# Kernel optimization log

Measured on AMD Instinct MI355X. Metric: run time of the kernel, lower is better.

The kernel has to match this reference:

```python
import jax, jax.numpy as jnp
import numpy as np

H = 16  # hidden size


def _gru_dir(x_tbi, Wih, Whh, bih, bhh, reverse):
    """Single-direction GRU over time. x_tbi: [T,B,I]. Returns [T,B,H] outputs
    aligned to original time positions (lax.scan reverse matches torch's
    bidirectional alignment). PyTorch gate order: r, z, n."""
    B = x_tbi.shape[1]
    h0 = jnp.zeros((B, Whh.shape[1]), x_tbi.dtype)
    # Precompute all input projections in one big GEMM: [T,B,3H]
    gi_all = jnp.einsum('tbi,gi->tbg', x_tbi, Wih) + bih

    def step(h, gi):
        gh = h @ Whh.T + bhh                     # [B,3H]
        i_r, i_z, i_n = jnp.split(gi, 3, axis=-1)
        h_r, h_z, h_n = jnp.split(gh, 3, axis=-1)
        r = jax.nn.sigmoid(i_r + h_r)
        z = jax.nn.sigmoid(i_z + h_z)
        n = jnp.tanh(i_n + r * h_n)
        h_new = (1.0 - z) * n + z * h
        return h_new, h_new

    _, ys = jax.lax.scan(step, h0, gi_all, reverse=reverse)
    return ys  # [T,B,H]


def _bigru_layer(x_tbi, pf, pb):
    yf = _gru_dir(x_tbi, pf[0], pf[1], pf[2], pf[3], False)
    yb = _gru_dir(x_tbi, pb[0], pb[1], pb[2], pb[3], True)
    return jnp.concatenate([yf, yb], axis=-1)  # [T,B,2H]


def setup_inputs() -> dict:
    key = jax.random.key(0)
    ks = jax.random.split(key, 20)
    B, T, I = 4096, 512, 1
    bound = 1.0 / np.sqrt(H)  # torch default init U(-1/sqrt(H), 1/sqrt(H))

    def u(k, shape):
        return jax.random.uniform(k, shape, jnp.float32, -bound, bound)

    inp = {'x': jax.random.normal(ks[0], (B, T, I), jnp.float32)}
    # layer 0: input dim 1; layer 1: input dim 2H=32. Suffix f=forward, b=backward.
    dims = {0: I, 1: 2 * H}
    i = 1
    for l in (0, 1):
        for d in ('f', 'b'):
            inp[f'W_ih_l{l}_{d}'] = u(ks[i], (3 * H, dims[l])); i += 1
            inp[f'W_hh_l{l}_{d}'] = u(ks[i], (3 * H, H)); i += 1
            inp[f'b_ih_l{l}_{d}'] = u(ks[i], (3 * H,)); i += 1
            inp[f'b_hh_l{l}_{d}'] = u(ks[i], (3 * H,)); i += 1
    return inp


def reference(x,
              W_ih_l0_f, W_hh_l0_f, b_ih_l0_f, b_hh_l0_f,
              W_ih_l0_b, W_hh_l0_b, b_ih_l0_b, b_hh_l0_b,
              W_ih_l1_f, W_hh_l1_f, b_ih_l1_f, b_hh_l1_f,
              W_ih_l1_b, W_hh_l1_b, b_ih_l1_b, b_hh_l1_b):
    x_tbi = jnp.transpose(x.astype(jnp.float32), (1, 0, 2))  # [T,B,1]
    y0 = _bigru_layer(x_tbi,
                      (W_ih_l0_f, W_hh_l0_f, b_ih_l0_f, b_hh_l0_f),
                      (W_ih_l0_b, W_hh_l0_b, b_ih_l0_b, b_hh_l0_b))
    y1 = _bigru_layer(y0,
                      (W_ih_l1_f, W_hh_l1_f, b_ih_l1_f, b_hh_l1_f),
                      (W_ih_l1_b, W_hh_l1_b, b_ih_l1_b, b_hh_l1_b))
    # out[:, -1, :] in batch_first layout == last time step of [T,B,2H]
    return y1[-1]  # [B, 2H]
```

## Files before the change

### kernel.cpp

```cpp
#include <hip/hip_runtime.h>
#include <hip/hip_fp16.h>

typedef float v2f __attribute__((ext_vector_type(2)));
typedef _Float16 h4t __attribute__((ext_vector_type(4)));
typedef _Float16 h8t __attribute__((ext_vector_type(8)));
typedef float f4t __attribute__((ext_vector_type(4)));

static constexpr int T = 512;
static constexpr int B = 4096;

__device__ __forceinline__ float frcp_(float x) { return __builtin_amdgcn_rcpf(x); }
__device__ __forceinline__ float sig_(float x) { return frcp_(1.0f + __expf(-x)); }
__device__ __forceinline__ float tanh_(float x) { return 1.0f - 2.0f * frcp_(1.0f + __expf(2.0f * x)); }

#define WAVE_SYNC() do { asm volatile("" ::: "memory"); \
                         __builtin_amdgcn_wave_barrier(); \
                         asm volatile("" ::: "memory"); } while (0)

__device__ __forceinline__ h4t pack4_(float a, float b, float c, float d) {
    auto p0 = __builtin_amdgcn_cvt_pkrtz(a, b);
    auto p1 = __builtin_amdgcn_cvt_pkrtz(c, d);
    union { struct { decltype(p0) a, b; } p; h4t h; } cv;
    cv.p.a = p0; cv.p.b = p1;
    return cv.h;
}

__global__ void __launch_bounds__(256, 2) k_l0(
    const float* __restrict__ x,
    const float* __restrict__ Wf, const float* __restrict__ Uf,
    const float* __restrict__ bif, const float* __restrict__ bhf,
    const float* __restrict__ Wb, const float* __restrict__ Ub,
    const float* __restrict__ bib, const float* __restrict__ bhb,
    __half* __restrict__ y0f,
    __half* __restrict__ y0b)
{
    __shared__ float hbuf[256];
    const int tid = threadIdx.x;
    const int j   = tid & 15;
    const int dir = (tid >> 4) & 1;
    const int s   = tid >> 5;
    const int b   = blockIdx.x * 8 + s;
    float* hb = hbuf + (tid >> 4) * 16;

    const float* Wih = dir ? Wb : Wf;
    const float* Whh = dir ? Ub : Uf;
    const float* bih = dir ? bib : bif;
    const float* bhh = dir ? bhb : bhf;

    v2f wr[8], wz[8], wn[8];
    {
        const v2f* pr = reinterpret_cast<const v2f*>(Whh + j * 16);
        const v2f* pz = reinterpret_cast<const v2f*>(Whh + (16 + j) * 16);
        const v2f* pn = reinterpret_cast<const v2f*>(Whh + (32 + j) * 16);
#pragma unroll
        for (int q = 0; q < 8; ++q) { wr[q] = pr[q]; wz[q] = pz[q]; wn[q] = pn[q]; }
    }
    const float wxr  = Wih[j], wxz = Wih[16 + j], wxn = Wih[32 + j];
    const float br   = bih[j] + bhh[j];
    const float bz   = bih[16 + j] + bhh[16 + j];
    const float bin_ = bih[32 + j];
    const float bhn  = bhh[32 + j];

    const int t0   = dir ? (T - 1) : 0;
    const int step = dir ? -1 : 1;
    const float* xp = x + (size_t)b * T + t0;
    __half* yp = (dir ? y0b : y0f) + ((size_t)t0 * B + b) * 16 + j;
    const ptrdiff_t ystep = (ptrdiff_t)step * B * 16;

    hb[j] = 0.0f;
    WAVE_SYNC();

    float xv = xp[0];
    float x1 = xp[step];
    const float* xq = xp + 2 * step;
    float hj = 0.0f;

    for (int it = 0; it < T; ++it) {
        float x2 = *xq;
        if (it < T - 3) xq += step;
        v2f A[8];
#pragma unroll
        for (int q = 0; q < 4; ++q) {
            float4 v = *reinterpret_cast<const float4*>(hb + 4 * q);
            A[2 * q + 0][0] = v.x; A[2 * q + 0][1] = v.y;
            A[2 * q + 1][0] = v.z; A[2 * q + 1][1] = v.w;
        }
        v2f a0 = { fmaf(xv, wxr, br), 0.0f };
        v2f a1 = { fmaf(xv, wxz, bz), 0.0f };
        v2f a2 = { bhn, 0.0f };
#pragma unroll
        for (int q = 0; q < 8; ++q) {
            a0 += wr[q] * A[q];
            a1 += wz[q] * A[q];
            a2 += wn[q] * A[q];
        }
        float ar = a0[0] + a0[1];
        float az = a1[0] + a1[1];
        float hn = a2[0] + a2[1];
        float r = sig_(ar), z = sig_(az);
        float n = tanh_(fmaf(r, hn, fmaf(xv, wxn, bin_)));
        hj = fmaf(z, hj - n, n);
        *yp = __float2half(hj);
        yp += ystep;
        WAVE_SYNC();
        hb[j] = hj;
        WAVE_SYNC();
        xv = x1; x1 = x2;
    }
}

__global__ void __launch_bounds__(64, 1) k_l1m(
    const __half* __restrict__ y0f, const __half* __restrict__ y0b,
    const float* __restrict__ Wih1, const float* __restrict__ Whh1,
    const float* __restrict__ bih1, const float* __restrict__ bhh1,
    const float* __restrict__ Wih1b,
    const float* __restrict__ bih1b, const float* __restrict__ bhh1b,
    float* __restrict__ out)
{
    const int lane = threadIdx.x & 63;
    const int c = lane & 15;
    const int g = lane >> 4;
    const int b = blockIdx.x * 16 + c;

    h8t Air, Aiz, Ain;
    {
        const float* pr = Wih1 + (size_t)c * 32 + 8 * g;
        const float* pz = Wih1 + (size_t)(16 + c) * 32 + 8 * g;
        const float* pn = Wih1 + (size_t)(32 + c) * 32 + 8 * g;
#pragma unroll
        for (int e = 0; e < 8; ++e) {
            Air[e] = (_Float16)pr[e];
            Aiz[e] = (_Float16)pz[e];
            Ain[e] = (_Float16)pn[e];
        }
    }
    h4t Ahr, Ahz, Ahn;
    {
        const float* pr = Whh1 + (size_t)c * 16 + 4 * g;
        const float* pz = Whh1 + (size_t)(16 + c) * 16 + 4 * g;
        const float* pn = Whh1 + (size_t)(32 + c) * 16 + 4 * g;
#pragma unroll
        for (int e = 0; e < 4; ++e) {
            Ahr[e] = (_Float16)pr[e];
            Ahz[e] = (_Float16)pz[e];
            Ahn[e] = (_Float16)pn[e];
        }
    }
    f4t Crb, Czb, Cnb, Chn, Z4;
#pragma unroll
    for (int i = 0; i < 4; ++i) {
        const int row = 4 * g + i;
        Crb[i] = bih1[row] + bhh1[row];
        Czb[i] = bih1[16 + row] + bhh1[16 + row];
        Cnb[i] = bih1[32 + row];
        Chn[i] = bhh1[32 + row];
        Z4[i]  = 0.0f;
    }

    const __half* ysrc = (g < 2) ? y0f : y0b;
    const uint4* yp = reinterpret_cast<const uint4*>(
        ysrc + (size_t)b * 16 + (size_t)(g & 1) * 8);
    const size_t ystr = (size_t)B * 2;

    uint4 ya  = yp[0];
    uint4 yb4 = yp[ystr];

    float h[4] = {0.0f, 0.0f, 0.0f, 0.0f};
    h4t Bh = {};

    for (int it = 0; it < T; ++it) {
        const size_t tn = (it < T - 2) ? (size_t)(it + 2) : (size_t)(T - 1);
        uint4 yc = yp[tn * ystr];
        h8t By;
        { union { uint4 u; h8t h; } cv; cv.u = ya; By = cv.h; }
        f4t Dr = __builtin_amdgcn_mfma_f32_16x16x32_f16(Air, By, Crb, 0, 0, 0);
        f4t Dz = __builtin_amdgcn_mfma_f32_16x16x32_f16(Aiz, By, Czb, 0, 0, 0);
        f4t Dn = __builtin_amdgcn_mfma_f32_16x16x32_f16(Ain, By, Cnb, 0, 0, 0);
        f4t Er = __builtin_amdgcn_mfma_f32_16x16x16f16(Ahr, Bh, Z4, 0, 0, 0);
        f4t Ez = __builtin_amdgcn_mfma_f32_16x16x16f16(Ahz, Bh, Z4, 0, 0, 0);
        f4t En = __builtin_amdgcn_mfma_f32_16x16x16f16(Ahn, Bh, Chn, 0, 0, 0);
#pragma unroll
        for (int i = 0; i < 4; ++i) {
            float r = sig_(Dr[i] + Er[i]);
            float z = sig_(Dz[i] + Ez[i]);
            float n = tanh_(fmaf(r, En[i], Dn[i]));
            h[i] = fmaf(z, h[i] - n, n);
        }
        Bh = pack4_(h[0], h[1], h[2], h[3]);
        ya = yb4; yb4 = yc;
    }

#pragma unroll
    for (int i = 0; i < 4; ++i)
        out[(size_t)b * 32 + 4 * g + i] = h[i];

    h8t Abr, Abz, Abn;
    {
        const float* pr = Wih1b + (size_t)c * 32 + 8 * g;
        const float* pz = Wih1b + (size_t)(16 + c) * 32 + 8 * g;
        const float* pn = Wih1b + (size_t)(32 + c) * 32 + 8 * g;
#pragma unroll
        for (int e = 0; e < 8; ++e) {
            Abr[e] = (_Float16)pr[e];
            Abz[e] = (_Float16)pz[e];
            Abn[e] = (_Float16)pn[e];
        }
    }
    f4t Cbr, Cbz, Cbn;
    float ghn[4];
#pragma unroll
    for (int i = 0; i < 4; ++i) {
        const int row = 4 * g + i;
        Cbr[i] = bih1b[row] + bhh1b[row];
        Cbz[i] = bih1b[16 + row] + bhh1b[16 + row];
        Cbn[i] = bih1b[32 + row];
        ghn[i] = bhh1b[32 + row];
    }
    h8t By;
    { union { uint4 u; h8t h; } cv; cv.u = ya; By = cv.h; }
    f4t Dr = __builtin_amdgcn_mfma_f32_16x16x32_f16(Abr, By, Cbr, 0, 0, 0);
    f4t Dz = __builtin_amdgcn_mfma_f32_16x16x32_f16(Abz, By, Cbz, 0, 0, 0);
    f4t Dn = __builtin_amdgcn_mfma_f32_16x16x32_f16(Abn, By, Cbn, 0, 0, 0);
#pragma unroll
    for (int i = 0; i < 4; ++i) {
        float r = sig_(Dr[i]);
        float z = sig_(Dz[i]);
        float n = tanh_(fmaf(r, ghn[i], Dn[i]));
        out[(size_t)b * 32 + 16 + 4 * g + i] = (1.0f - z) * n;
    }
}

extern "C" void kernel_launch(void* const* d_in, const int* in_sizes, int n_in,
                              void* d_out, int out_size, void* d_ws, size_t ws_size,
                              hipStream_t stream) {
    const float* x     = (const float*)d_in[0];
    const float* Wih0f = (const float*)d_in[1];
    const float* Whh0f = (const float*)d_in[2];
    const float* bih0f = (const float*)d_in[3];
    const float* bhh0f = (const float*)d_in[4];
    const float* Wih0b = (const float*)d_in[5];
    const float* Whh0b = (const float*)d_in[6];
    const float* bih0b = (const float*)d_in[7];
    const float* bhh0b = (const float*)d_in[8];
    const float* Wih1f = (const float*)d_in[9];
    const float* Whh1f = (const float*)d_in[10];
    const float* bih1f = (const float*)d_in[11];
    const float* bhh1f = (const float*)d_in[12];
    const float* Wih1b = (const float*)d_in[13];
    const float* bih1b = (const float*)d_in[15];
    const float* bhh1b = (const float*)d_in[16];

    __half* y0f = (__half*)d_ws;
    __half* y0b = y0f + (size_t)T * B * 16;
    float* out = (float*)d_out;

    hipLaunchKernelGGL(k_l0, dim3(B * 2 / 16), dim3(256), 0, stream,
                       x, Wih0f, Whh0f, bih0f, bhh0f,
                       Wih0b, Whh0b, bih0b, bhh0b, y0f, y0b);
    hipLaunchKernelGGL(k_l1m, dim3(B / 16), dim3(64), 0, stream,
                       y0f, y0b, Wih1f, Whh1f, bih1f, bhh1f,
                       Wih1b, bih1b, bhh1b, out);
}
```

Before: 287.6 us.

## Rewrite layer-0 GRU recurrence to use MFMA with fp16 hidden state

The layer-0 kernel no longer computes the recurrent matvec per thread from an LDS-shared hidden state. Each wave now handles 16 batch columns of one direction and runs three 16x16x16 fp16 MFMAs per step, with the hidden state packed to fp16 as the B operand. This removes LDS traffic and the wave barriers in the serial loop, and mirrors the existing layer-1 MFMA kernel. In exchange the recurrent weights and hidden state are rounded to fp16, and each step now has MFMA latency on its dependency chain.

```diff
diff --git a/kernel.cpp b/kernel.cpp
--- a/kernel.cpp
+++ b/kernel.cpp
@@ -1,7 +1,6 @@
 #include <hip/hip_runtime.h>
 #include <hip/hip_fp16.h>
 
-typedef float v2f __attribute__((ext_vector_type(2)));
 typedef _Float16 h4t __attribute__((ext_vector_type(4)));
 typedef _Float16 h8t __attribute__((ext_vector_type(8)));
 typedef float f4t __attribute__((ext_vector_type(4)));
@@ -12,10 +11,6 @@
 __device__ __forceinline__ float frcp_(float x) { return __builtin_amdgcn_rcpf(x); }
 __device__ __forceinline__ float sig_(float x) { return frcp_(1.0f + __expf(-x)); }
 __device__ __forceinline__ float tanh_(float x) { return 1.0f - 2.0f * frcp_(1.0f + __expf(2.0f * x)); }
-
-#define WAVE_SYNC() do { asm volatile("" ::: "memory"); \
-                         __builtin_amdgcn_wave_barrier(); \
-                         asm volatile("" ::: "memory"); } while (0)
 
 __device__ __forceinline__ h4t pack4_(float a, float b, float c, float d) {
     auto p0 = __builtin_amdgcn_cvt_pkrtz(a, b);
@@ -25,7 +20,7 @@
     return cv.h;
 }
 
-__global__ void __launch_bounds__(256, 2) k_l0(
+__global__ void __launch_bounds__(64, 1) k_l0m(
     const float* __restrict__ x,
     const float* __restrict__ Wf, const float* __restrict__ Uf,
     const float* __restrict__ bif, const float* __restrict__ bhf,
@@ -34,78 +29,73 @@
     __half* __restrict__ y0f,
     __half* __restrict__ y0b)
 {
-    __shared__ float hbuf[256];
-    const int tid = threadIdx.x;
-    const int j   = tid & 15;
-    const int dir = (tid >> 4) & 1;
-    const int s   = tid >> 5;
-    const int b   = blockIdx.x * 8 + s;
-    float* hb = hbuf + (tid >> 4) * 16;
+    const int lane = threadIdx.x & 63;
+    const int c = lane & 15;
+    const int g = lane >> 4;
+    const int dir = blockIdx.x >> 8;
+    const int b = (blockIdx.x & 255) * 16 + c;
 
     const float* Wih = dir ? Wb : Wf;
     const float* Whh = dir ? Ub : Uf;
     const float* bih = dir ? bib : bif;
     const float* bhh = dir ? bhb : bhf;
 
-    v2f wr[8], wz[8], wn[8];
-    {
-        const v2f* pr = reinterpret_cast<const v2f*>(Whh + j * 16);
-        const v2f* pz = reinterpret_cast<const v2f*>(Whh + (16 + j) * 16);
-        const v2f* pn = reinterpret_cast<const v2f*>(Whh + (32 + j) * 16);
-#pragma unroll
-        for (int q = 0; q < 8; ++q) { wr[q] = pr[q]; wz[q] = pz[q]; wn[q] = pn[q]; }
-    }
-    const float wxr  = Wih[j], wxz = Wih[16 + j], wxn = Wih[32 + j];
-    const float br   = bih[j] + bhh[j];
-    const float bz   = bih[16 + j] + bhh[16 + j];
-    const float bin_ = bih[32 + j];
-    const float bhn  = bhh[32 + j];
+    h4t Ahr, Ahz, Ahn;
+#pragma unroll
+    for (int e = 0; e < 4; ++e) {
+        Ahr[e] = (_Float16)Whh[(size_t)c * 16 + 4 * g + e];
+        Ahz[e] = (_Float16)Whh[(size_t)(16 + c) * 16 + 4 * g + e];
+        Ahn[e] = (_Float16)Whh[(size_t)(32 + c) * 16 + 4 * g + e];
+    }
+    float wxr[4], wxz[4], wxn[4], br_[4], bz_[4], bin_[4];
+    f4t Chn;
+#pragma unroll
+    for (int i = 0; i < 4; ++i) {
+        const int row = 4 * g + i;
+        wxr[i] = Wih[row];
+        wxz[i] = Wih[16 + row];
+        wxn[i] = Wih[32 + row];
+        br_[i] = bih[row] + bhh[row];
+        bz_[i] = bih[16 + row] + bhh[16 + row];
+        bin_[i] = bih[32 + row];
+        Chn[i] = bhh[32 + row];
+    }
 
     const int t0   = dir ? (T - 1) : 0;
     const int step = dir ? -1 : 1;
     const float* xp = x + (size_t)b * T + t0;
-    __half* yp = (dir ? y0b : y0f) + ((size_t)t0 * B + b) * 16 + j;
+    __half* yp = (dir ? y0b : y0f) + ((size_t)t0 * B + b) * 16 + 4 * g;
     const ptrdiff_t ystep = (ptrdiff_t)step * B * 16;
 
-    hb[j] = 0.0f;
-    WAVE_SYNC();
-
-    float xv = xp[0];
-    float x1 = xp[step];
+    float xa = xp[0];
+    float xb1 = xp[step];
     const float* xq = xp + 2 * step;
-    float hj = 0.0f;
+    float h[4] = {0.0f, 0.0f, 0.0f, 0.0f};
+    h4t Bh = {};
 
     for (int it = 0; it < T; ++it) {
         float x2 = *xq;
         if (it < T - 3) xq += step;
-        v2f A[8];
-#pragma unroll
-        for (int q = 0; q < 4; ++q) {
-            float4 v = *reinterpret_cast<const float4*>(hb + 4 * q);
-            A[2 * q + 0][0] = v.x; A[2 * q + 0][1] = v.y;
-            A[2 * q + 1][0] = v.z; A[2 * q + 1][1] = v.w;
-        }
-        v2f a0 = { fmaf(xv, wxr, br), 0.0f };
-        v2f a1 = { fmaf(xv, wxz, bz), 0.0f };
-        v2f a2 = { bhn, 0.0f };
-#pragma unroll
-        for (int q = 0; q < 8; ++q) {
-            a0 += wr[q] * A[q];
-            a1 += wz[q] * A[q];
-            a2 += wn[q] * A[q];
-        }
-        float ar = a0[0] + a0[1];
-        float az = a1[0] + a1[1];
-        float hn = a2[0] + a2[1];
-        float r = sig_(ar), z = sig_(az);
-        float n = tanh_(fmaf(r, hn, fmaf(xv, wxn, bin_)));
-        hj = fmaf(z, hj - n, n);
-        *yp = __float2half(hj);
+        f4t Cr, Cz;
+#pragma unroll
+        for (int i = 0; i < 4; ++i) {
+            Cr[i] = fmaf(xa, wxr[i], br_[i]);
+            Cz[i] = fmaf(xa, wxz[i], bz_[i]);
+        }
+        f4t Er = __builtin_amdgcn_mfma_f32_16x16x16f16(Ahr, Bh, Cr, 0, 0, 0);
+        f4t Ez = __builtin_amdgcn_mfma_f32_16x16x16f16(Ahz, Bh, Cz, 0, 0, 0);
+        f4t En = __builtin_amdgcn_mfma_f32_16x16x16f16(Ahn, Bh, Chn, 0, 0, 0);
+#pragma unroll
+        for (int i = 0; i < 4; ++i) {
+            float r = sig_(Er[i]);
+            float z = sig_(Ez[i]);
+            float n = tanh_(fmaf(r, En[i], fmaf(xa, wxn[i], bin_[i])));
+            h[i] = fmaf(z, h[i] - n, n);
+        }
+        Bh = pack4_(h[0], h[1], h[2], h[3]);
+        *reinterpret_cast<h4t*>(yp) = Bh;
         yp += ystep;
-        WAVE_SYNC();
-        hb[j] = hj;
-        WAVE_SYNC();
-        xv = x1; x1 = x2;
+        xa = xb1; xb1 = x2;
     }
 }
 
@@ -254,7 +244,7 @@
     __half* y0b = y0f + (size_t)T * B * 16;
     float* out = (float*)d_out;
 
-    hipLaunchKernelGGL(k_l0, dim3(B * 2 / 16), dim3(256), 0, stream,
+    hipLaunchKernelGGL(k_l0m, dim3(512), dim3(64), 0, stream,
                        x, Wih0f, Whh0f, bih0f, bhh0f,
                        Wih0b, Whh0b, bih0b, bhh0b, y0f, y0b);
     hipLaunchKernelGGL(k_l1m, dim3(B / 16), dim3(64), 0, stream,
```

Result: slower. 371.4 us (+29.2%).
